# Kernel optimization log

Hardware: AMD Instinct MI355X
Metric: run time of the kernel (lower is better)

Reference implementation:

```python
import jax, jax.numpy as jnp
import numpy as np

LORA_DIM = 16          # hard-coded in module
LORA_TOKEN_INDEX = 1   # lora_dim*layer_sequence + 1 with layer_sequence=0
B, S, D, H = 4, 2048, 1024, 4096  # num_hiddens = 4*num_input (forced by view())


def setup_inputs() -> dict:
    key = jax.random.key(0)
    ks = jax.random.split(key, 6)
    x = jax.random.normal(ks[0], (B, S, D), dtype=jnp.float32)
    W1 = jax.random.normal(ks[1], (H, D), dtype=jnp.float32) * 0.02
    b1 = jnp.zeros((H,), dtype=jnp.float32)
    W2 = jax.random.normal(ks[2], (D, H), dtype=jnp.float32) * 0.02
    b2 = jnp.zeros((D,), dtype=jnp.float32)
    scale = jnp.asarray(0.001, dtype=jnp.float32)  # nn.Parameter(torch.tensor(0.001))
    return {"x": x, "W1": W1, "b1": b1, "W2": W2, "b2": b2, "scale": scale}


def reference(x, W1, b1, W2, b2, scale):
    Bx, Sx, Dx = x.shape
    Hx = W1.shape[0]  # = 4*Dx
    # 16 lora tokens starting at LORA_TOKEN_INDEX
    lt = jax.lax.dynamic_slice_in_dim(x, LORA_TOKEN_INDEX, LORA_DIM, axis=1)
    even = lt[:, ::2, :]  # (B, 8, D)
    odd = lt[:, 1::2, :]  # (B, 8, D)
    # per-sample low-rank weight updates:
    # result_multiplication[b,k] = outer(even[b,k], odd[b,k]) (D,D)
    # matrix1 = first 4 blocks stacked -> (B, 4D, D); matrix2 = last 4 reshaped -> (B, D, 4D)
    m1 = (even[:, :4, :, None] * odd[:, :4, None, :]).reshape(Bx, Hx, Dx)
    m2 = (even[:, 4:, :, None] * odd[:, 4:, None, :]).reshape(Bx, Dx, Hx)
    # x @ (W1 + scale*m1)^T + b1, fused without repeating W1 per batch
    h = jnp.einsum('bsd,hd->bsh', x, W1) + scale * jnp.einsum('bsd,bhd->bsh', x, m1) + b1
    h = jax.nn.gelu(h, approximate=False)  # torch nn.GELU default = exact erf
    out = jnp.einsum('bsh,oh->bso', h, W2) + scale * jnp.einsum('bsh,boh->bso', h, m2) + b2
    return out
```

## Files before the change

kernel.cpp:

```cpp
#include <hip/hip_runtime.h>
#include <cstdint>
#include <cstddef>

#define MROWS 8192
#define DDIM  1024
#define HDIM  4096

typedef __bf16 bf16x8 __attribute__((ext_vector_type(8)));
typedef float  f32x4  __attribute__((ext_vector_type(4)));

typedef __attribute__((address_space(1))) void* as1_vp;
typedef __attribute__((address_space(3))) void* as3_vp;

__device__ __forceinline__ unsigned short f2bf(float f) {
  unsigned int u = __builtin_bit_cast(unsigned int, f);
  u += 0x7fffu + ((u >> 16) & 1u);
  return (unsigned short)(u >> 16);
}
__device__ __forceinline__ float bf2f(unsigned short h) {
  return __builtin_bit_cast(float, (unsigned int)h << 16);
}

__device__ __forceinline__ float fast_gelu(float x) {
  float x3 = x * x * x;
  float z = 0.7978845608028654f * x + 0.03567740814f * x3;
  float e = __builtin_amdgcn_exp2f(z * 2.8853900817779268f);
  float t = 1.0f - 2.0f * __builtin_amdgcn_rcpf(e + 1.0f);
  return 0.5f * x * (1.0f + t);
}

__device__ __forceinline__ void gld_lds16(const unsigned short* g, unsigned short* lds) {
  __builtin_amdgcn_global_load_lds((as1_vp)(uintptr_t)g, (as3_vp)lds, 16, 0, 0);
}

__global__ __launch_bounds__(256) void pre_kernel(
    const float* __restrict__ x, const float* __restrict__ w1,
    const float* __restrict__ w2, unsigned short* __restrict__ xb,
    unsigned short* __restrict__ w1b, unsigned short* __restrict__ w2b,
    float* __restrict__ p1) {
  if (blockIdx.x < 8192) {
    int i = blockIdx.x * 256 + threadIdx.x;
    const float* src; unsigned short* dst; int off;
    if (i < 1048576) { src = w1; dst = w1b; off = i; }
    else             { src = w2; dst = w2b; off = i - 1048576; }
    float4 v = ((const float4*)src)[off];
    ushort4 o;
    o.x = f2bf(v.x); o.y = f2bf(v.y); o.z = f2bf(v.z); o.w = f2bf(v.w);
    ((ushort4*)dst)[off] = o;
    return;
  }
  const int bid = blockIdx.x - 8192;
  const int wave = threadIdx.x >> 6, lane = threadIdx.x & 63;
  const int m = bid * 4 + wave;
  const int b = m >> 11;
  const float4* xrow4 = (const float4*)(x + (size_t)m * DDIM);
  const float4* od4   = (const float4*)(x + ((size_t)b * 2048 + 2) * DDIM);
  ushort4* xbrow4 = (ushort4*)(xb + (size_t)m * DDIM);
  float a0 = 0.f, a1 = 0.f, a2 = 0.f, a3 = 0.f;
#pragma unroll
  for (int it = 0; it < 4; ++it) {
    int g = it * 64 + lane;
    float4 v = xrow4[g];
    ushort4 o; o.x = f2bf(v.x); o.y = f2bf(v.y); o.z = f2bf(v.z); o.w = f2bf(v.w);
    xbrow4[g] = o;
    float4 o0 = od4[g];
    float4 o1 = od4[512 + g];
    float4 o2 = od4[1024 + g];
    float4 o3 = od4[1536 + g];
    a0 += v.x * o0.x + v.y * o0.y + v.z * o0.z + v.w * o0.w;
    a1 += v.x * o1.x + v.y * o1.y + v.z * o1.z + v.w * o1.w;
    a2 += v.x * o2.x + v.y * o2.y + v.z * o2.z + v.w * o2.w;
    a3 += v.x * o3.x + v.y * o3.y + v.z * o3.z + v.w * o3.w;
  }
#pragma unroll
  for (int off = 32; off > 0; off >>= 1) {
    a0 += __shfl_down(a0, off);
    a1 += __shfl_down(a1, off);
    a2 += __shfl_down(a2, off);
    a3 += __shfl_down(a3, off);
  }
  if (lane == 0) {
    float4 r; r.x = a0; r.y = a1; r.z = a2; r.w = a3;
    ((float4*)p1)[m] = r;
  }
}

#define VMW(n) asm volatile("s_waitcnt vmcnt(" #n ")" ::: "memory")
#define LKW()  asm volatile("s_waitcnt lgkmcnt(0)" ::: "memory")
#define BAR()  asm volatile("s_barrier" ::: "memory")

__global__ __launch_bounds__(512, 2) void gemm1_kernel(
    const unsigned short* __restrict__ xb, const unsigned short* __restrict__ w1b,
    const float* __restrict__ x, const float* __restrict__ b1,
    const float* __restrict__ p1, const float* __restrict__ scale_p,
    unsigned short* __restrict__ hact) {
  __shared__ __align__(16) unsigned short As[4 * 256 * 32];
  __shared__ __align__(16) unsigned short Bs[4 * 256 * 32];

  const int id = blockIdx.x;
  const int xcd = id & 7, w = id >> 3;
  const int m0 = (xcd * 4 + (w & 3)) * 256;
  const int n0 = (w >> 2) * 256;

  const int tid  = threadIdx.x;
  const int wave = tid >> 6, lane = tid & 63;
  const int quad = lane >> 4, l16 = lane & 15;
  const int wm2  = wave >> 2;
  const int wn2  = wave & 3;

  const unsigned short *gA0, *gA1, *gB0, *gB1;
  {
    int idx = tid;
    int r = idx >> 2, sl = idx & 3, c = (sl - (r >> 1)) & 3;
    gA0 = xb  + (size_t)(m0 + r) * DDIM + c * 8;
    gB0 = w1b + (size_t)(n0 + r) * DDIM + c * 8;
    idx = 512 + tid;
    r = idx >> 2; sl = idx & 3; c = (sl - (r >> 1)) & 3;
    gA1 = xb  + (size_t)(m0 + r) * DDIM + c * 8;
    gB1 = w1b + (size_t)(n0 + r) * DDIM + c * 8;
  }
  const int ldsOff0 = (wave * 64) * 8;
  const int ldsOff1 = (512 + wave * 64) * 8;

#define STAGE1(tt, sb) do {                                   \
    const int _k = (tt) * 32;                                 \
    unsigned short* _a = &As[(sb) * 8192];                    \
    unsigned short* _b = &Bs[(sb) * 8192];                    \
    gld_lds16(gA0 + _k, _a + ldsOff0);                        \
    gld_lds16(gA1 + _k, _a + ldsOff1);                        \
    gld_lds16(gB0 + _k, _b + ldsOff0);                        \
    gld_lds16(gB1 + _k, _b + ldsOff1);                        \
  } while (0)

  f32x4 acc[8][4];
  const f32x4 z = {0.f, 0.f, 0.f, 0.f};
#pragma unroll
  for (int i = 0; i < 8; ++i)
#pragma unroll
    for (int j = 0; j < 4; ++j) acc[i][j] = z;

  auto compute_tile = [&](const unsigned short* __restrict__ Ab,
                          const unsigned short* __restrict__ Bb) {
    bf16x8 a[8], b[4];
#pragma unroll
    for (int j = 0; j < 4; ++j) {
      const int rb = wn2 * 64 + j * 16 + l16;
      b[j] = *(const bf16x8*)(Bb + rb * 32 + ((quad + (rb >> 1)) & 3) * 8);
    }
#pragma unroll
    for (int i = 0; i < 8; ++i) {
      const int ra = wm2 * 128 + i * 16 + l16;
      a[i] = *(const bf16x8*)(Ab + ra * 32 + ((quad + (ra >> 1)) & 3) * 8);
    }
    __builtin_amdgcn_s_setprio(1);
#pragma unroll
    for (int i = 0; i < 8; ++i)
#pragma unroll
      for (int j = 0; j < 4; ++j)
        acc[i][j] = __builtin_amdgcn_mfma_f32_16x16x32_bf16(a[i], b[j], acc[i][j], 0, 0, 0);
    __builtin_amdgcn_s_setprio(0);
  };

#define TILE_FULL(tt, cb, sb) do {                            \
    STAGE1((tt) + 3, sb);                                     \
    VMW(12);                                                  \
    BAR();                                                    \
    compute_tile(&As[(cb) * 8192], &Bs[(cb) * 8192]);         \
    LKW();                                                    \
    BAR();                                                    \
  } while (0)

  STAGE1(0, 0);
  STAGE1(1, 1);
  STAGE1(2, 2);

#pragma unroll 1
  for (int t = 0; t < 28; t += 4) {
    TILE_FULL(t + 0, 0, 3);
    TILE_FULL(t + 1, 1, 0);
    TILE_FULL(t + 2, 2, 1);
    TILE_FULL(t + 3, 3, 2);
  }
  TILE_FULL(28, 0, 3);
  VMW(8);  BAR(); compute_tile(&As[1 * 8192], &Bs[1 * 8192]);
  VMW(4);  BAR(); compute_tile(&As[2 * 8192], &Bs[2 * 8192]);
  VMW(0);  BAR(); compute_tile(&As[3 * 8192], &Bs[3 * 8192]);

  const float sc = scale_p[0];
  const int bidx = m0 >> 11;
  const int i1 = (n0 + wn2 * 64) >> 10;
  const float* exrow = x + ((size_t)(bidx * 2048 + 1 + 2 * i1)) * DDIM;

  float exv[4], b1v[4]; int nn[4];
#pragma unroll
  for (int j = 0; j < 4; ++j) {
    nn[j]  = n0 + wn2 * 64 + j * 16 + l16;
    exv[j] = exrow[nn[j] & 1023];
    b1v[j] = b1[nn[j]];
  }
#pragma unroll
  for (int i = 0; i < 8; ++i) {
#pragma unroll
    for (int r = 0; r < 4; ++r) {
      const int m = m0 + wm2 * 128 + i * 16 + quad * 4 + r;
      const float pv = p1[(size_t)m * 4 + i1] * sc;
#pragma unroll
      for (int j = 0; j < 4; ++j) {
        float v = acc[i][j][r] + b1v[j] + pv * exv[j];
        hact[(size_t)m * HDIM + nn[j]] = f2bf(fast_gelu(v));
      }
    }
  }
#undef TILE_FULL
#undef STAGE1
}

__global__ __launch_bounds__(256) void gemm2_kernel(
    const unsigned short* __restrict__ hact, const unsigned short* __restrict__ w2b,
    const float* __restrict__ x, const float* __restrict__ b2,
    const float* __restrict__ scale_p, float* __restrict__ out) {
  __shared__ __align__(16) unsigned short As[128 * 128];
  __shared__ __align__(16) unsigned short Bs[128 * 128];
  __shared__ __align__(16) unsigned short od_lds[1024];
  __shared__ __align__(16) float p2s[128 * 4];
  const int id = blockIdx.x;
  const int xcd = id & 7, w = id >> 3;
  const int m0 = (xcd * 8 + (w >> 3)) * 128;
  const int n0 = (w & 7) * 128;
  const int tid = threadIdx.x;
  const int wave = tid >> 6, lane = tid & 63, quad = lane >> 4, l16 = lane & 15;
  const int wm = (wave >> 1) * 64, wn = (wave & 1) * 64;
  const int bidx = m0 >> 11;
  const int i2 = n0 >> 8;

  {
    const float4* src = (const float4*)(x + ((size_t)(bidx * 2048 + 10 + 2 * i2)) * DDIM);
    float4 v = src[tid];
    ushort4 o; o.x = f2bf(v.x); o.y = f2bf(v.y); o.z = f2bf(v.z); o.w = f2bf(v.w);
    ((ushort4*)od_lds)[tid] = o;
  }

  f32x4 acc[4][4];
  const f32x4 z = {0.f, 0.f, 0.f, 0.f};
#pragma unroll
  for (int i = 0; i < 4; ++i)
#pragma unroll
    for (int j = 0; j < 4; ++j) acc[i][j] = z;
  f32x4 pacc[4] = {z, z, z, z};
  const bf16x8 zer8 = __builtin_bit_cast(bf16x8, z);

  const unsigned short* ga[8]; const unsigned short* gb[8];
#pragma unroll
  for (int s = 0; s < 8; ++s) {
    int idx = wave * 512 + s * 64 + lane;
    int r = idx >> 4, sl = idx & 15;
    int c = (sl - r) & 15;
    ga[s] = hact + (size_t)(m0 + r) * HDIM + c * 8;
    gb[s] = w2b  + (size_t)(n0 + r) * HDIM + c * 8;
  }

  for (int k0 = 0; k0 < HDIM; k0 += 128) {
    __syncthreads();
#pragma unroll
    for (int s = 0; s < 8; ++s) gld_lds16(ga[s] + k0, As + (wave * 8 + s) * 512);
#pragma unroll
    for (int s = 0; s < 8; ++s) gld_lds16(gb[s] + k0, Bs + (wave * 8 + s) * 512);
    __syncthreads();
    const int odbase = k0 & 1023;
#pragma unroll
    for (int kk = 0; kk < 128; kk += 32) {
      bf16x8 a[4], b[4];
      const int cbase = (kk >> 3) + quad;
#pragma unroll
      for (int i = 0; i < 4; ++i) {
        const int ra = wm + i * 16 + l16;
        const int rb = wn + i * 16 + l16;
        a[i] = *(const bf16x8*)(As + ra * 128 + ((cbase + ra) & 15) * 8);
        b[i] = *(const bf16x8*)(Bs + rb * 128 + ((cbase + rb) & 15) * 8);
      }
      if (wn == 0) {
        bf16x8 odv = *(const bf16x8*)(od_lds + odbase + kk + quad * 8);
        bf16x8 bod = (l16 == 0) ? odv : zer8;
#pragma unroll
        for (int i = 0; i < 4; ++i)
          pacc[i] = __builtin_amdgcn_mfma_f32_16x16x32_bf16(a[i], bod, pacc[i], 0, 0, 0);
      }
#pragma unroll
      for (int i = 0; i < 4; ++i)
#pragma unroll
        for (int j = 0; j < 4; ++j)
          acc[i][j] = __builtin_amdgcn_mfma_f32_16x16x32_bf16(a[i], b[j], acc[i][j], 0, 0, 0);
    }
    if (((k0 + 128) & 1023) == 0) {
      const int seg = k0 >> 10;
      if (wn == 0) {
        if (l16 == 0) {
#pragma unroll
          for (int i = 0; i < 4; ++i)
#pragma unroll
            for (int e = 0; e < 4; ++e)
              p2s[(wm + i * 16 + quad * 4 + e) * 4 + seg] = pacc[i][e];
        }
#pragma unroll
        for (int i = 0; i < 4; ++i) pacc[i] = z;
      }
    }
  }
  __syncthreads();

  const float sc = scale_p[0];
  const float* evrow = x + ((size_t)(bidx * 2048 + 9 + 2 * i2)) * DDIM;

  float4 ev[4]; float b2v[4]; int nn[4];
#pragma unroll
  for (int j = 0; j < 4; ++j) {
    nn[j] = n0 + wn + j * 16 + l16;
    ev[j]  = *(const float4*)(evrow + 4 * (nn[j] & 255));
    b2v[j] = b2[nn[j]];
  }
#pragma unroll
  for (int i = 0; i < 4; ++i) {
#pragma unroll
    for (int r = 0; r < 4; ++r) {
      const int mloc = wm + i * 16 + quad * 4 + r;
      const int m = m0 + mloc;
      const float4 pv = *(const float4*)(p2s + mloc * 4);
#pragma unroll
      for (int j = 0; j < 4; ++j) {
        float lora = ev[j].x * pv.x + ev[j].y * pv.y + ev[j].z * pv.z + ev[j].w * pv.w;
        out[(size_t)m * DDIM + nn[j]] = acc[i][j][r] + b2v[j] + sc * lora;
      }
    }
  }
}

extern "C" void kernel_launch(void* const* d_in, const int* in_sizes, int n_in,
                              void* d_out, int out_size, void* d_ws, size_t ws_size,
                              hipStream_t stream) {
  const float* x     = (const float*)d_in[0];
  const float* W1    = (const float*)d_in[1];
  const float* b1    = (const float*)d_in[2];
  const float* W2    = (const float*)d_in[3];
  const float* b2    = (const float*)d_in[4];
  const float* scale = (const float*)d_in[5];
  float* out = (float*)d_out;

  char* ws = (char*)d_ws;
  unsigned short* xb   = (unsigned short*)(ws);
  unsigned short* w1b  = (unsigned short*)(ws + 16777216);
  unsigned short* w2b  = (unsigned short*)(ws + 25165824);
  unsigned short* hact = (unsigned short*)(ws + 33554432);
  float*          p1   = (float*)(ws + 100663296);

  pre_kernel<<<dim3(10240), dim3(256), 0, stream>>>(x, W1, W2, xb, w1b, w2b, p1);
  gemm1_kernel<<<dim3(512), dim3(512), 0, stream>>>(xb, w1b, x, b1, p1, scale, hact);
  gemm2_kernel<<<dim3(512), dim3(256), 0, stream>>>(hact, w2b, x, b2, scale, out);
}
```

Before: 266.4 us.

## Shrink gemm1 tiles and software-pipeline both GEMMs with register double-buffering

gemm1 moves from 256x256 tiles with 512 threads to 128x128 tiles with 256 threads and four times as many blocks. Both GEMMs now use a 4-deep LDS ring fed by global_load_lds, plus ping-pong register fragments, so the LDS reads for the next k-slice are issued right after the MFMAs of the current one. gemm2 switches from 128-wide k chunks with syncthreads to 32-wide stages and splits the lora side-accumulation across both column waves. The aim is to hide load latency and cut barrier stalls, at the cost of less data reuse per block in gemm1 and more complex synchronisation.

```diff
diff --git a/kernel.cpp b/kernel.cpp
--- a/kernel.cpp
+++ b/kernel.cpp
@@ -16,9 +16,6 @@
   unsigned int u = __builtin_bit_cast(unsigned int, f);
   u += 0x7fffu + ((u >> 16) & 1u);
   return (unsigned short)(u >> 16);
-}
-__device__ __forceinline__ float bf2f(unsigned short h) {
-  return __builtin_bit_cast(float, (unsigned int)h << 16);
 }
 
 __device__ __forceinline__ float fast_gelu(float x) {
@@ -32,6 +29,11 @@
 __device__ __forceinline__ void gld_lds16(const unsigned short* g, unsigned short* lds) {
   __builtin_amdgcn_global_load_lds((as1_vp)(uintptr_t)g, (as3_vp)lds, 16, 0, 0);
 }
+
+#define VMW(n)  asm volatile("s_waitcnt vmcnt(" #n ")" ::: "memory")
+#define LKW()   asm volatile("s_waitcnt lgkmcnt(0)" ::: "memory")
+#define BAR()   asm volatile("s_barrier" ::: "memory")
+#define SB0()   __builtin_amdgcn_sched_barrier(0)
 
 __global__ __launch_bounds__(256) void pre_kernel(
     const float* __restrict__ x, const float* __restrict__ w1,
@@ -85,28 +87,24 @@
   }
 }
 
-#define VMW(n) asm volatile("s_waitcnt vmcnt(" #n ")" ::: "memory")
-#define LKW()  asm volatile("s_waitcnt lgkmcnt(0)" ::: "memory")
-#define BAR()  asm volatile("s_barrier" ::: "memory")
-
-__global__ __launch_bounds__(512, 2) void gemm1_kernel(
+__global__ __launch_bounds__(256, 2) void gemm1_kernel(
     const unsigned short* __restrict__ xb, const unsigned short* __restrict__ w1b,
     const float* __restrict__ x, const float* __restrict__ b1,
     const float* __restrict__ p1, const float* __restrict__ scale_p,
     unsigned short* __restrict__ hact) {
-  __shared__ __align__(16) unsigned short As[4 * 256 * 32];
-  __shared__ __align__(16) unsigned short Bs[4 * 256 * 32];
+  __shared__ __align__(16) unsigned short As[4 * 4096];
+  __shared__ __align__(16) unsigned short Bs[4 * 4096];
 
   const int id = blockIdx.x;
   const int xcd = id & 7, w = id >> 3;
-  const int m0 = (xcd * 4 + (w & 3)) * 256;
-  const int n0 = (w >> 2) * 256;
+  const int m0 = (xcd * 8 + (w & 7)) * 128;
+  const int n0 = (w >> 3) * 128;
 
   const int tid  = threadIdx.x;
   const int wave = tid >> 6, lane = tid & 63;
   const int quad = lane >> 4, l16 = lane & 15;
-  const int wm2  = wave >> 2;
-  const int wn2  = wave & 3;
+  const int wm2  = (wave >> 1) * 64;
+  const int wn2  = (wave & 1) * 64;
 
   const unsigned short *gA0, *gA1, *gB0, *gB1;
   {
@@ -114,95 +112,100 @@
     int r = idx >> 2, sl = idx & 3, c = (sl - (r >> 1)) & 3;
     gA0 = xb  + (size_t)(m0 + r) * DDIM + c * 8;
     gB0 = w1b + (size_t)(n0 + r) * DDIM + c * 8;
-    idx = 512 + tid;
+    idx = 256 + tid;
     r = idx >> 2; sl = idx & 3; c = (sl - (r >> 1)) & 3;
     gA1 = xb  + (size_t)(m0 + r) * DDIM + c * 8;
     gB1 = w1b + (size_t)(n0 + r) * DDIM + c * 8;
   }
-  const int ldsOff0 = (wave * 64) * 8;
-  const int ldsOff1 = (512 + wave * 64) * 8;
-
-#define STAGE1(tt, sb) do {                                   \
+  const int ldsO0 = wave * 512;
+  const int ldsO1 = 2048 + wave * 512;
+
+#define STG1(tt, bb) do {                                     \
     const int _k = (tt) * 32;                                 \
-    unsigned short* _a = &As[(sb) * 8192];                    \
-    unsigned short* _b = &Bs[(sb) * 8192];                    \
-    gld_lds16(gA0 + _k, _a + ldsOff0);                        \
-    gld_lds16(gA1 + _k, _a + ldsOff1);                        \
-    gld_lds16(gB0 + _k, _b + ldsOff0);                        \
-    gld_lds16(gB1 + _k, _b + ldsOff1);                        \
+    unsigned short* _a = As + (bb) * 4096;                    \
+    unsigned short* _b = Bs + (bb) * 4096;                    \
+    gld_lds16(gA0 + _k, _a + ldsO0);                          \
+    gld_lds16(gA1 + _k, _a + ldsO1);                          \
+    gld_lds16(gB0 + _k, _b + ldsO0);                          \
+    gld_lds16(gB1 + _k, _b + ldsO1);                          \
   } while (0)
 
-  f32x4 acc[8][4];
+  f32x4 acc[4][4];
   const f32x4 z = {0.f, 0.f, 0.f, 0.f};
 #pragma unroll
-  for (int i = 0; i < 8; ++i)
+  for (int i = 0; i < 4; ++i)
 #pragma unroll
     for (int j = 0; j < 4; ++j) acc[i][j] = z;
 
-  auto compute_tile = [&](const unsigned short* __restrict__ Ab,
-                          const unsigned short* __restrict__ Bb) {
-    bf16x8 a[8], b[4];
+  bf16x8 aA[4], bA[4], aB[4], bB[4];
+
+  auto RD = [&](int nb, bf16x8 (&aa)[4], bf16x8 (&bb)[4]) {
+    const unsigned short* Ab = As + nb * 4096;
+    const unsigned short* Bb = Bs + nb * 4096;
 #pragma unroll
     for (int j = 0; j < 4; ++j) {
-      const int rb = wn2 * 64 + j * 16 + l16;
-      b[j] = *(const bf16x8*)(Bb + rb * 32 + ((quad + (rb >> 1)) & 3) * 8);
-    }
-#pragma unroll
-    for (int i = 0; i < 8; ++i) {
-      const int ra = wm2 * 128 + i * 16 + l16;
-      a[i] = *(const bf16x8*)(Ab + ra * 32 + ((quad + (ra >> 1)) & 3) * 8);
-    }
+      const int rb = wn2 + j * 16 + l16;
+      bb[j] = *(const bf16x8*)(Bb + rb * 32 + ((quad + (rb >> 1)) & 3) * 8);
+    }
+#pragma unroll
+    for (int i = 0; i < 4; ++i) {
+      const int ra = wm2 + i * 16 + l16;
+      aa[i] = *(const bf16x8*)(Ab + ra * 32 + ((quad + (ra >> 1)) & 3) * 8);
+    }
+  };
+  auto MF = [&](bf16x8 (&aa)[4], bf16x8 (&bb)[4]) {
     __builtin_amdgcn_s_setprio(1);
 #pragma unroll
-    for (int i = 0; i < 8; ++i)
+    for (int i = 0; i < 4; ++i)
 #pragma unroll
       for (int j = 0; j < 4; ++j)
-        acc[i][j] = __builtin_amdgcn_mfma_f32_16x16x32_bf16(a[i], b[j], acc[i][j], 0, 0, 0);
+        acc[i][j] = __builtin_amdgcn_mfma_f32_16x16x32_bf16(aa[i], bb[j], acc[i][j], 0, 0, 0);
     __builtin_amdgcn_s_setprio(0);
   };
 
-#define TILE_FULL(tt, cb, sb) do {                            \
-    STAGE1((tt) + 3, sb);                                     \
-    VMW(12);                                                  \
-    BAR();                                                    \
-    compute_tile(&As[(cb) * 8192], &Bs[(cb) * 8192]);         \
-    LKW();                                                    \
-    BAR();                                                    \
+#define G1BODY(tt, SB, NB, CUR, NXT) do {                     \
+    STG1((tt) + 3, SB);                                       \
+    LKW(); SB0();                                             \
+    MF(a##CUR, b##CUR);                                       \
+    VMW(8); BAR();                                            \
+    RD(NB, a##NXT, b##NXT);                                   \
   } while (0)
 
-  STAGE1(0, 0);
-  STAGE1(1, 1);
-  STAGE1(2, 2);
+  STG1(0, 0);
+  STG1(1, 1);
+  STG1(2, 2);
+  VMW(8); BAR();
+  RD(0, aA, bA);
 
 #pragma unroll 1
   for (int t = 0; t < 28; t += 4) {
-    TILE_FULL(t + 0, 0, 3);
-    TILE_FULL(t + 1, 1, 0);
-    TILE_FULL(t + 2, 2, 1);
-    TILE_FULL(t + 3, 3, 2);
-  }
-  TILE_FULL(28, 0, 3);
-  VMW(8);  BAR(); compute_tile(&As[1 * 8192], &Bs[1 * 8192]);
-  VMW(4);  BAR(); compute_tile(&As[2 * 8192], &Bs[2 * 8192]);
-  VMW(0);  BAR(); compute_tile(&As[3 * 8192], &Bs[3 * 8192]);
+    G1BODY(t + 0, 3, 1, A, B);
+    G1BODY(t + 1, 0, 2, B, A);
+    G1BODY(t + 2, 1, 3, A, B);
+    G1BODY(t + 3, 2, 0, B, A);
+  }
+  G1BODY(28, 3, 1, A, B);
+  LKW(); SB0(); MF(aB, bB); VMW(4); BAR(); RD(2, aA, bA);
+  LKW(); SB0(); MF(aA, bA); VMW(0); BAR(); RD(3, aB, bB);
+  LKW(); SB0(); MF(aB, bB);
 
   const float sc = scale_p[0];
   const int bidx = m0 >> 11;
-  const int i1 = (n0 + wn2 * 64) >> 10;
+  const int i1 = (n0 + wn2) >> 10;
   const float* exrow = x + ((size_t)(bidx * 2048 + 1 + 2 * i1)) * DDIM;
 
   float exv[4], b1v[4]; int nn[4];
 #pragma unroll
   for (int j = 0; j < 4; ++j) {
-    nn[j]  = n0 + wn2 * 64 + j * 16 + l16;
+    nn[j]  = n0 + wn2 + j * 16 + l16;
     exv[j] = exrow[nn[j] & 1023];
     b1v[j] = b1[nn[j]];
   }
 #pragma unroll
-  for (int i = 0; i < 8; ++i) {
+  for (int i = 0; i < 4; ++i) {
 #pragma unroll
     for (int r = 0; r < 4; ++r) {
-      const int m = m0 + wm2 * 128 + i * 16 + quad * 4 + r;
+      const int m = m0 + wm2 + i * 16 + quad * 4 + r;
       const float pv = p1[(size_t)m * 4 + i1] * sc;
 #pragma unroll
       for (int j = 0; j < 4; ++j) {
@@ -211,25 +214,28 @@
       }
     }
   }
-#undef TILE_FULL
-#undef STAGE1
-}
-
-__global__ __launch_bounds__(256) void gemm2_kernel(
+#undef G1BODY
+#undef STG1
+}
+
+__global__ __launch_bounds__(256, 2) void gemm2_kernel(
     const unsigned short* __restrict__ hact, const unsigned short* __restrict__ w2b,
     const float* __restrict__ x, const float* __restrict__ b2,
     const float* __restrict__ scale_p, float* __restrict__ out) {
-  __shared__ __align__(16) unsigned short As[128 * 128];
-  __shared__ __align__(16) unsigned short Bs[128 * 128];
+  __shared__ __align__(16) unsigned short As[4 * 4096];
+  __shared__ __align__(16) unsigned short Bs[4 * 4096];
   __shared__ __align__(16) unsigned short od_lds[1024];
   __shared__ __align__(16) float p2s[128 * 4];
+
   const int id = blockIdx.x;
   const int xcd = id & 7, w = id >> 3;
-  const int m0 = (xcd * 8 + (w >> 3)) * 128;
-  const int n0 = (w & 7) * 128;
+  const int m0 = (xcd * 8 + (w & 7)) * 128;
+  const int n0 = (w >> 3) * 128;
   const int tid = threadIdx.x;
   const int wave = tid >> 6, lane = tid & 63, quad = lane >> 4, l16 = lane & 15;
-  const int wm = (wave >> 1) * 64, wn = (wave & 1) * 64;
+  const int wm2 = (wave >> 1) * 64;
+  const int wn2 = (wave & 1) * 64;
+  const bool hi = (wave & 1);
   const int bidx = m0 >> 11;
   const int i2 = n0 >> 8;
 
@@ -239,6 +245,7 @@
     ushort4 o; o.x = f2bf(v.x); o.y = f2bf(v.y); o.z = f2bf(v.z); o.w = f2bf(v.w);
     ((ushort4*)od_lds)[tid] = o;
   }
+  LKW();
 
   f32x4 acc[4][4];
   const f32x4 z = {0.f, 0.f, 0.f, 0.f};
@@ -246,67 +253,106 @@
   for (int i = 0; i < 4; ++i)
 #pragma unroll
     for (int j = 0; j < 4; ++j) acc[i][j] = z;
-  f32x4 pacc[4] = {z, z, z, z};
+  f32x4 pacc[2] = {z, z};
   const bf16x8 zer8 = __builtin_bit_cast(bf16x8, z);
 
-  const unsigned short* ga[8]; const unsigned short* gb[8];
-#pragma unroll
-  for (int s = 0; s < 8; ++s) {
-    int idx = wave * 512 + s * 64 + lane;
-    int r = idx >> 4, sl = idx & 15;
-    int c = (sl - r) & 15;
-    ga[s] = hact + (size_t)(m0 + r) * HDIM + c * 8;
-    gb[s] = w2b  + (size_t)(n0 + r) * HDIM + c * 8;
-  }
-
-  for (int k0 = 0; k0 < HDIM; k0 += 128) {
-    __syncthreads();
-#pragma unroll
-    for (int s = 0; s < 8; ++s) gld_lds16(ga[s] + k0, As + (wave * 8 + s) * 512);
-#pragma unroll
-    for (int s = 0; s < 8; ++s) gld_lds16(gb[s] + k0, Bs + (wave * 8 + s) * 512);
-    __syncthreads();
-    const int odbase = k0 & 1023;
-#pragma unroll
-    for (int kk = 0; kk < 128; kk += 32) {
-      bf16x8 a[4], b[4];
-      const int cbase = (kk >> 3) + quad;
-#pragma unroll
-      for (int i = 0; i < 4; ++i) {
-        const int ra = wm + i * 16 + l16;
-        const int rb = wn + i * 16 + l16;
-        a[i] = *(const bf16x8*)(As + ra * 128 + ((cbase + ra) & 15) * 8);
-        b[i] = *(const bf16x8*)(Bs + rb * 128 + ((cbase + rb) & 15) * 8);
-      }
-      if (wn == 0) {
-        bf16x8 odv = *(const bf16x8*)(od_lds + odbase + kk + quad * 8);
-        bf16x8 bod = (l16 == 0) ? odv : zer8;
-#pragma unroll
-        for (int i = 0; i < 4; ++i)
-          pacc[i] = __builtin_amdgcn_mfma_f32_16x16x32_bf16(a[i], bod, pacc[i], 0, 0, 0);
-      }
-#pragma unroll
-      for (int i = 0; i < 4; ++i)
-#pragma unroll
-        for (int j = 0; j < 4; ++j)
-          acc[i][j] = __builtin_amdgcn_mfma_f32_16x16x32_bf16(a[i], b[j], acc[i][j], 0, 0, 0);
-    }
-    if (((k0 + 128) & 1023) == 0) {
-      const int seg = k0 >> 10;
-      if (wn == 0) {
-        if (l16 == 0) {
-#pragma unroll
-          for (int i = 0; i < 4; ++i)
-#pragma unroll
-            for (int e = 0; e < 4; ++e)
-              p2s[(wm + i * 16 + quad * 4 + e) * 4 + seg] = pacc[i][e];
-        }
-#pragma unroll
-        for (int i = 0; i < 4; ++i) pacc[i] = z;
-      }
-    }
-  }
-  __syncthreads();
+  const unsigned short *gA0, *gA1, *gB0, *gB1;
+  {
+    int idx = tid;
+    int r = idx >> 2, sl = idx & 3, c = (sl - (r >> 1)) & 3;
+    gA0 = hact + (size_t)(m0 + r) * HDIM + c * 8;
+    gB0 = w2b  + (size_t)(n0 + r) * HDIM + c * 8;
+    idx = 256 + tid;
+    r = idx >> 2; sl = idx & 3; c = (sl - (r >> 1)) & 3;
+    gA1 = hact + (size_t)(m0 + r) * HDIM + c * 8;
+    gB1 = w2b  + (size_t)(n0 + r) * HDIM + c * 8;
+  }
+  const int ldsO0 = wave * 512;
+  const int ldsO1 = 2048 + wave * 512;
+
+#define STG2(tt, bb) do {                                     \
+    const int _k = (tt) * 32;                                 \
+    unsigned short* _a = As + (bb) * 4096;                    \
+    unsigned short* _b = Bs + (bb) * 4096;                    \
+    gld_lds16(gA0 + _k, _a + ldsO0);                          \
+    gld_lds16(gA1 + _k, _a + ldsO1);                          \
+    gld_lds16(gB0 + _k, _b + ldsO0);                          \
+    gld_lds16(gB1 + _k, _b + ldsO1);                          \
+  } while (0)
+
+  bf16x8 aA[4], bA[4], odA;
+  bf16x8 aB[4], bB[4], odB;
+
+  auto RD2 = [&](int nb, int tt1, bf16x8 (&aa)[4], bf16x8 (&bb)[4], bf16x8& ov) {
+    ov = *(const bf16x8*)(od_lds + ((tt1 * 32) & 1023) + quad * 8);
+    const unsigned short* Ab = As + nb * 4096;
+    const unsigned short* Bb = Bs + nb * 4096;
+#pragma unroll
+    for (int j = 0; j < 4; ++j) {
+      const int rb = wn2 + j * 16 + l16;
+      bb[j] = *(const bf16x8*)(Bb + rb * 32 + ((quad + (rb >> 1)) & 3) * 8);
+    }
+#pragma unroll
+    for (int i = 0; i < 4; ++i) {
+      const int ra = wm2 + i * 16 + l16;
+      aa[i] = *(const bf16x8*)(Ab + ra * 32 + ((quad + (ra >> 1)) & 3) * 8);
+    }
+  };
+  auto MF2 = [&](bf16x8 (&aa)[4], bf16x8 (&bb)[4], bf16x8& ov) {
+    bf16x8 bod = (l16 == 0) ? ov : zer8;
+    bf16x8 pa0 = hi ? aa[2] : aa[0];
+    bf16x8 pa1 = hi ? aa[3] : aa[1];
+    pacc[0] = __builtin_amdgcn_mfma_f32_16x16x32_bf16(pa0, bod, pacc[0], 0, 0, 0);
+    pacc[1] = __builtin_amdgcn_mfma_f32_16x16x32_bf16(pa1, bod, pacc[1], 0, 0, 0);
+    __builtin_amdgcn_s_setprio(1);
+#pragma unroll
+    for (int i = 0; i < 4; ++i)
+#pragma unroll
+      for (int j = 0; j < 4; ++j)
+        acc[i][j] = __builtin_amdgcn_mfma_f32_16x16x32_bf16(aa[i], bb[j], acc[i][j], 0, 0, 0);
+    __builtin_amdgcn_s_setprio(0);
+  };
+  auto flush_p2 = [&](int seg) {
+    const int ibase = hi ? 2 : 0;
+    if (l16 == 0) {
+#pragma unroll
+      for (int ip = 0; ip < 2; ++ip)
+#pragma unroll
+        for (int e = 0; e < 4; ++e)
+          p2s[(wm2 + (ibase + ip) * 16 + quad * 4 + e) * 4 + seg] = pacc[ip][e];
+    }
+    pacc[0] = z; pacc[1] = z;
+  };
+
+#define G2BODY(tt, SB, NB, CUR, NXT) do {                     \
+    STG2((tt) + 3, SB);                                       \
+    LKW(); SB0();                                             \
+    MF2(a##CUR, b##CUR, od##CUR);                             \
+    if (((tt) & 31) == 31) flush_p2((tt) >> 5);               \
+    VMW(8); BAR();                                            \
+    RD2(NB, (tt) + 1, a##NXT, b##NXT, od##NXT);               \
+  } while (0)
+
+  STG2(0, 0);
+  STG2(1, 1);
+  STG2(2, 2);
+  VMW(8); BAR();
+  RD2(0, 0, aA, bA, odA);
+
+#pragma unroll 1
+  for (int t = 0; t < 124; t += 4) {
+    G2BODY(t + 0, 3, 1, A, B);
+    G2BODY(t + 1, 0, 2, B, A);
+    G2BODY(t + 2, 1, 3, A, B);
+    G2BODY(t + 3, 2, 0, B, A);
+  }
+  G2BODY(124, 3, 1, A, B);
+  LKW(); SB0(); MF2(aB, bB, odB); VMW(4); BAR(); RD2(2, 126, aA, bA, odA);
+  LKW(); SB0(); MF2(aA, bA, odA); VMW(0); BAR(); RD2(3, 127, aB, bB, odB);
+  LKW(); SB0(); MF2(aB, bB, odB);
+  flush_p2(3);
+  LKW();
+  BAR();
 
   const float sc = scale_p[0];
   const float* evrow = x + ((size_t)(bidx * 2048 + 9 + 2 * i2)) * DDIM;
@@ -314,7 +360,7 @@
   float4 ev[4]; float b2v[4]; int nn[4];
 #pragma unroll
   for (int j = 0; j < 4; ++j) {
-    nn[j] = n0 + wn + j * 16 + l16;
+    nn[j] = n0 + wn2 + j * 16 + l16;
     ev[j]  = *(const float4*)(evrow + 4 * (nn[j] & 255));
     b2v[j] = b2[nn[j]];
   }
@@ -322,7 +368,7 @@
   for (int i = 0; i < 4; ++i) {
 #pragma unroll
     for (int r = 0; r < 4; ++r) {
-      const int mloc = wm + i * 16 + quad * 4 + r;
+      const int mloc = wm2 + i * 16 + quad * 4 + r;
       const int m = m0 + mloc;
       const float4 pv = *(const float4*)(p2s + mloc * 4);
 #pragma unroll
@@ -332,6 +378,8 @@
       }
     }
   }
+#undef G2BODY
+#undef STG2
 }
 
 extern "C" void kernel_launch(void* const* d_in, const int* in_sizes, int n_in,
@@ -353,6 +401,6 @@
   float*          p1   = (float*)(ws + 100663296);
 
   pre_kernel<<<dim3(10240), dim3(256), 0, stream>>>(x, W1, W2, xb, w1b, w2b, p1);
-  gemm1_kernel<<<dim3(512), dim3(512), 0, stream>>>(xb, w1b, x, b1, p1, scale, hact);
+  gemm1_kernel<<<dim3(2048), dim3(256), 0, stream>>>(xb, w1b, x, b1, p1, scale, hact);
   gemm2_kernel<<<dim3(512), dim3(256), 0, stream>>>(hact, w2b, x, b2, scale, out);
 }
```

Result: slower. 282.3 us (+6.0%).
